# Kernel tuning notes

Hardware: AMD Instinct MI355X
Metric: run time of the kernel (lower is better)

## Reference

```python
import jax, jax.numpy as jnp
import numpy as np

NUM_HEADS = 16
KEY_DIM = 64
D_MODEL = 1024  # input feature dim


def setup_inputs() -> dict:
    key = jax.random.key(0)
    ks = jax.random.split(key, 10)
    B, T = 2, 2048
    s = 0.02
    return {
        "query": jax.random.normal(ks[0], (B, T, D_MODEL), jnp.float32),
        "Wq": jax.random.normal(ks[1], (D_MODEL, NUM_HEADS * KEY_DIM), jnp.float32) * s,
        "bq": jnp.zeros((NUM_HEADS * KEY_DIM,), jnp.float32),
        "Wk": jax.random.normal(ks[2], (D_MODEL, KEY_DIM), jnp.float32) * s,
        "bk": jnp.zeros((KEY_DIM,), jnp.float32),
        "Wv": jax.random.normal(ks[3], (D_MODEL, KEY_DIM), jnp.float32) * s,
        "bv": jnp.zeros((KEY_DIM,), jnp.float32),
        "Wo": jax.random.normal(ks[4], (NUM_HEADS * KEY_DIM, NUM_HEADS * KEY_DIM), jnp.float32) * s,
        "bo": jnp.zeros((NUM_HEADS * KEY_DIM,), jnp.float32),
    }


def reference(query, Wq, bq, Wk, bk, Wv, bv, Wo, bo):
    B, Tq, _ = query.shape
    # self-attention: key = value = query
    q = query @ Wq + bq                      # [B,Tq,H*D]
    k = query @ Wk + bk                      # [B,Tk,D] (single shared head)
    v = query @ Wv + bv                      # [B,Tk,D]
    q = q.reshape(B, Tq, NUM_HEADS, KEY_DIM)
    # scores: [B,H,Tq,Tk] — K broadcast across heads (MQA)
    scores = jnp.einsum("bqhd,bkd->bhqk", q, k) / jnp.sqrt(
        jnp.asarray(KEY_DIM, jnp.float32))
    attn = jax.nn.softmax(scores, axis=-1)
    out = jnp.einsum("bhqk,bkd->bqhd", attn, v)  # [B,Tq,H,D]
    out = out.reshape(B, Tq, NUM_HEADS * KEY_DIM)
    return out @ Wo + bo
```

## Files before the change

### kernel.cpp

```cpp
#include <hip/hip_runtime.h>
#include <math.h>

#define T_SEQ 2048
#define DM 1024
#define NH 16
#define KD 64
#define MTOT 4096

typedef __attribute__((ext_vector_type(16))) float f32x16;
typedef __attribute__((ext_vector_type(8))) __bf16 bf16x8;
typedef __attribute__((ext_vector_type(4))) __bf16 bf16x4;
typedef __attribute__((ext_vector_type(2))) __bf16 bf16x2;
typedef __attribute__((ext_vector_type(2))) int i32x2;

#define MFMA32 __builtin_amdgcn_mfma_f32_32x32x16_bf16

#define QSCALE 0.1803368801111f

__global__ void detect_dtype(const unsigned short* __restrict__ w, int* flag) {
  __shared__ int s;
  if (threadIdx.x == 0) s = 0;
  __syncthreads();
  int bad = 0;
  for (int i = threadIdx.x; i < 4096; i += blockDim.x) {
    unsigned e = (w[i] >> 7) & 0xFF;
    if (e >= 0xC0) bad = 1;
  }
  if (bad) atomicOr(&s, 1);
  __syncthreads();
  if (threadIdx.x == 0) *flag = s;
}

template <typename T> struct alignas(4 * sizeof(T)) V4T { T v[4]; };

template <typename T>
__device__ __forceinline__ float4 ld4f(const T* p) {
  V4T<T> g = *reinterpret_cast<const V4T<T>*>(p);
  return make_float4((float)g.v[0], (float)g.v[1], (float)g.v[2], (float)g.v[3]);
}

struct bf2 { __bf16 h, l; };
__device__ __forceinline__ bf2 split2(float v) {
  bf2 r;
  r.h = (__bf16)v;
  r.l = (__bf16)(v - (float)r.h);
  return r;
}

__device__ __forceinline__ unsigned pkbf(__bf16 a, __bf16 b) {
  bf16x2 t;
  t[0] = a;
  t[1] = b;
  return __builtin_bit_cast(unsigned, t);
}

__device__ __forceinline__ float fexp2(float x) {
#if __has_builtin(__builtin_amdgcn_exp2f)
  return __builtin_amdgcn_exp2f(x);
#else
  return __expf(0.69314718056f * x);
#endif
}

__device__ __forceinline__ void plswap(unsigned& a, unsigned& b) {
  i32x2 r = __builtin_amdgcn_permlane32_swap((int)a, (int)b, false, false);
  a = (unsigned)r[0];
  b = (unsigned)r[1];
}

__device__ __forceinline__ f32x16 zero16() {
  f32x16 z;
#pragma unroll
  for (int i = 0; i < 16; ++i) z[i] = 0.f;
  return z;
}

__device__ __forceinline__ int drow(int reg, int l5) {
  return (reg & 3) + 8 * (reg >> 2) + 4 * l5;
}

__device__ __forceinline__ void gload16(const void* g, void* l) {
  __builtin_amdgcn_global_load_lds(
      (const __attribute__((address_space(1))) unsigned int*)g,
      (__attribute__((address_space(3))) unsigned int*)l, 16, 0, 0);
}

__device__ __forceinline__ int swzc(int row, int c) {
  return (((((c >> 3) ^ row) & 7)) << 3) | (c & 7);
}

template <typename T, bool LO>
__global__ __launch_bounds__(256) void asplit(
    const int* __restrict__ flag, int want, const T* __restrict__ A,
    __bf16* __restrict__ Ah, __bf16* __restrict__ Al) {
  if (*flag != want) return;
  const int gid = blockIdx.x * 256 + threadIdx.x;
  const int row = gid >> 7;
  const int c0 = (gid & 127) * 8;
  float4 v0 = ld4f(A + (size_t)row * 1024 + c0);
  float4 v1 = ld4f(A + (size_t)row * 1024 + c0 + 4);
  float vv[8] = {v0.x, v0.y, v0.z, v0.w, v1.x, v1.y, v1.z, v1.w};
  bf16x8 h, lo;
#pragma unroll
  for (int j = 0; j < 8; ++j) {
    bf2 s = split2(vv[j]);
    h[j] = s.h;
    lo[j] = s.l;
  }
  const int cb = (c0 & ~63) | (swzc(row & 7, c0 & 63) & ~7);
  *reinterpret_cast<bf16x8*>(Ah + (size_t)row * 1024 + cb) = h;
  if (LO) *reinterpret_cast<bf16x8*>(Al + (size_t)row * 1024 + cb) = lo;
}

template <typename T, bool LO>
__global__ __launch_bounds__(256) void tsplit(
    const int* __restrict__ flag, int want, const T* __restrict__ W,
    __bf16* __restrict__ Th, __bf16* __restrict__ Tl, int K, int N) {
  if (*flag != want) return;
  __shared__ float ts[32][33];
  const int t = threadIdx.x;
  const int k0 = blockIdx.x * 32, n0 = blockIdx.y * 32;
#pragma unroll
  for (int i = 0; i < 4; ++i) {
    int idx = t + 256 * i;
    int r = idx >> 5, c = idx & 31;
    ts[r][c] = (float)W[(size_t)(k0 + r) * N + n0 + c];
  }
  __syncthreads();
#pragma unroll
  for (int i = 0; i < 4; ++i) {
    int idx = t + 256 * i;
    int r = idx >> 5, c = idx & 31;
    bf2 s = split2(ts[c][r]);
    const int rr = n0 + r, cc = k0 + c;
    const int sc = (cc & ~63) | swzc(rr & 7, cc & 63);
    Th[(size_t)rr * K + sc] = s.h;
    if (LO) Tl[(size_t)rr * K + sc] = s.l;
  }
}

template <typename T>
__global__ __launch_bounds__(256, 4) void gemmqkv(
    const int* __restrict__ flag, int want,
    const __bf16* __restrict__ Ah_g, const __bf16* __restrict__ Bh_g,
    const T* __restrict__ bq, const T* __restrict__ bk,
    const T* __restrict__ bv,
    __bf16* __restrict__ Qh, __bf16* __restrict__ Kh2,
    __bf16* __restrict__ Vh2) {
  if (*flag != want) return;
  __shared__ __bf16 As[128][64], Bs[128][64];
  const int t = threadIdx.x, l = t & 63, w = t >> 6;
  const int l31 = l & 31, l5 = l >> 5, l7 = l31 & 7;
  const int m0 = blockIdx.x * 128, n0 = blockIdx.y * 128;

  f32x16 acc[4];
#pragma unroll
  for (int nt = 0; nt < 4; ++nt) acc[nt] = zero16();

  for (int k0 = 0; k0 < 1024; k0 += 64) {
    __syncthreads();
#pragma unroll
    for (int i = 0; i < 4; ++i) {
      const int idx = i * 256 + t;
      const int rr = idx >> 3;
      const int c8 = (t & 7) * 8;
      gload16(Ah_g + (size_t)(m0 + rr) * 1024 + k0 + c8, (__bf16*)As + idx * 8);
      gload16(Bh_g + (size_t)(n0 + rr) * 1024 + k0 + c8, (__bf16*)Bs + idx * 8);
    }
    __syncthreads();
#pragma unroll
    for (int kb = 0; kb < 4; ++kb) {
      const int p = ((2 * kb + l5) ^ l7) * 8;
      bf16x8 ah = *reinterpret_cast<const bf16x8*>(&As[w * 32 + l31][p]);
#pragma unroll
      for (int nt = 0; nt < 4; ++nt) {
        bf16x8 bh = *reinterpret_cast<const bf16x8*>(&Bs[nt * 32 + l31][p]);
        acc[nt] = MFMA32(ah, bh, acc[nt], 0, 0, 0);
      }
    }
  }
#pragma unroll
  for (int nt = 0; nt < 4; ++nt) {
    const int cbase = n0 + nt * 32;
    const int col = cbase + l31;
    if (cbase < 1024) {
      const float bb = (float)bq[col];
#pragma unroll
      for (int reg = 0; reg < 16; ++reg) {
        const int mrow = m0 + w * 32 + drow(reg, l5);
        Qh[(size_t)mrow * 1024 + col] = (__bf16)((acc[nt][reg] + bb) * QSCALE);
      }
    } else if (cbase < 1088) {
      const int d = col - 1024;
      const float bb = (float)bk[d];
#pragma unroll
      for (int reg = 0; reg < 16; ++reg) {
        const int mrow = m0 + w * 32 + drow(reg, l5);
        Kh2[(size_t)mrow * 64 + swzc(mrow & 7, d)] = (__bf16)(acc[nt][reg] + bb);
      }
    } else {
      const int d = col - 1088;
      const float bb = (float)bv[d];
#pragma unroll
      for (int reg = 0; reg < 16; ++reg) {
        const int mrow = m0 + w * 32 + drow(reg, l5);
        const int bb2 = mrow >> 11, tt = mrow & 2047;
        const int sct = (tt & ~63) | swzc(d & 7, tt & 63);
        Vh2[((size_t)bb2 * 64 + d) * 2048 + sct] = (__bf16)(acc[nt][reg] + bb);
      }
    }
  }
}

template <typename T>
__global__ __launch_bounds__(256, 2) void gemmwo(
    const int* __restrict__ flag, int want,
    const __bf16* __restrict__ Ahi, const __bf16* __restrict__ Alo,
    const __bf16* __restrict__ Bh, const __bf16* __restrict__ Bl,
    const T* __restrict__ bias, T* __restrict__ CT) {
  if (*flag != want) return;
  __shared__ __bf16 Ah[128][64], Al[128][64];
  __shared__ __bf16 Bth[128][64], Btl[128][64];
  const int t = threadIdx.x, l = t & 63, w = t >> 6;
  const int l31 = l & 31, l5 = l >> 5, l7 = l31 & 7;
  const int m0 = blockIdx.x * 128, n0 = blockIdx.y * 128;

  f32x16 acc[4];
#pragma unroll
  for (int nt = 0; nt < 4; ++nt) acc[nt] = zero16();

  for (int k0 = 0; k0 < 1024; k0 += 64) {
    __syncthreads();
#pragma unroll
    for (int i = 0; i < 4; ++i) {
      const int idx = i * 256 + t;
      const int rr = idx >> 3;
      const int c8 = (t & 7) * 8;
      const size_t ga = (size_t)(m0 + rr) * 1024 + k0 + c8;
      gload16(Ahi + ga, (__bf16*)Ah + idx * 8);
      gload16(Alo + ga, (__bf16*)Al + idx * 8);
      const size_t gb = (size_t)(n0 + rr) * 1024 + k0 + c8;
      gload16(Bh + gb, (__bf16*)Bth + idx * 8);
      gload16(Bl + gb, (__bf16*)Btl + idx * 8);
    }
    __syncthreads();
#pragma unroll
    for (int kb = 0; kb < 4; ++kb) {
      const int p = ((2 * kb + l5) ^ l7) * 8;
      bf16x8 ah = *reinterpret_cast<const bf16x8*>(&Ah[w * 32 + l31][p]);
      bf16x8 al = *reinterpret_cast<const bf16x8*>(&Al[w * 32 + l31][p]);
#pragma unroll
      for (int nt = 0; nt < 4; ++nt) {
        bf16x8 bh = *reinterpret_cast<const bf16x8*>(&Bth[nt * 32 + l31][p]);
        bf16x8 bl = *reinterpret_cast<const bf16x8*>(&Btl[nt * 32 + l31][p]);
        acc[nt] = MFMA32(al, bh, acc[nt], 0, 0, 0);
        acc[nt] = MFMA32(ah, bl, acc[nt], 0, 0, 0);
        acc[nt] = MFMA32(ah, bh, acc[nt], 0, 0, 0);
      }
    }
  }
#pragma unroll
  for (int nt = 0; nt < 4; ++nt) {
    const int col = n0 + nt * 32 + l31;
    const float bb = (float)bias[col];
#pragma unroll
    for (int reg = 0; reg < 16; ++reg) {
      const int mrow = m0 + w * 32 + drow(reg, l5);
      CT[(size_t)mrow * 1024 + col] = (T)(acc[nt][reg] + bb);
    }
  }
}

template <typename T>
__global__ __launch_bounds__(512, 2) void attn8(
    const int* __restrict__ flag, int want,
    const __bf16* __restrict__ Qh_g, const __bf16* __restrict__ Kh_g,
    const __bf16* __restrict__ Vh_g,
    __bf16* __restrict__ AOhi, __bf16* __restrict__ AOlo) {
  if (*flag != want) return;
  __shared__ alignas(16) char arena[67584];
  const int t = threadIdx.x, l = t & 63, w = t >> 6;
  const int wq = w & 3, kvh = w >> 2;
  const int l31 = l & 31, l5 = l >> 5, l7 = l31 & 7;
  const int tl = t & 255;
  const int q0 = blockIdx.x * 256;
  const int h = blockIdx.y, b = blockIdx.z;

  __bf16* Kbase = (__bf16*)(arena + kvh * 16384);
  __bf16* Vbase = (__bf16*)(arena + 32768 + kvh * 16384);

  bf16x8 qh0[4], qh1[4];
  {
    const size_t qa = ((size_t)(b * T_SEQ + q0 + wq * 64 + l31)) * DM + h * KD;
#pragma unroll
    for (int ks = 0; ks < 4; ++ks) {
      qh0[ks] = *reinterpret_cast<const bf16x8*>(Qh_g + qa + ks * 16 + l5 * 8);
      qh1[ks] = *reinterpret_cast<const bf16x8*>(Qh_g + qa + (size_t)32 * DM + ks * 16 + l5 * 8);
    }
  }

  f32x16 o0 = zero16(), o1 = zero16(), o2 = zero16(), o3 = zero16();
  float lsa = 0.f, lsb = 0.f;

  const __bf16* Kg = Kh_g + (size_t)b * T_SEQ * KD;
  const __bf16* Vg = Vh_g + (size_t)b * KD * T_SEQ;
  const int sc8 = (tl & 7) * 8;
  const int kbase = kvh * 1024;

#define ASTAGE(BUF, KT0)                                                       \
  {                                                                            \
    const int r0 = tl >> 3, r1 = (256 + tl) >> 3;                              \
    gload16(Kg + (size_t)((KT0) + r0) * KD + sc8, Kbase + (BUF)*4096 + tl * 8);\
    gload16(Kg + (size_t)((KT0) + r1) * KD + sc8,                              \
            Kbase + (BUF)*4096 + (256 + tl) * 8);                              \
    gload16(Vg + (size_t)r0 * T_SEQ + (KT0) + sc8, Vbase + (BUF)*4096 + tl * 8);\
    gload16(Vg + (size_t)r1 * T_SEQ + (KT0) + sc8,                             \
            Vbase + (BUF)*4096 + (256 + tl) * 8);                              \
  }

  ASTAGE(0, kbase);
  __syncthreads();
  int cur = 0;

  for (int kt = 0; kt < 1024; kt += 64) {
    if (kt + 64 < 1024) ASTAGE(cur ^ 1, kbase + kt + 64);

    float rsa = 0.f, rsb = 0.f;
#pragma unroll
    for (int hf = 0; hf < 2; ++hf) {
      f32x16 sva = zero16(), svb = zero16();
#pragma unroll
      for (int ks = 0; ks < 4; ++ks) {
        const int p = ((2 * ks + l5) ^ l7) * 8;
        bf16x8 kh = *reinterpret_cast<const bf16x8*>(
            Kbase + cur * 4096 + (hf * 32 + l31) * 64 + p);
        sva = MFMA32(kh, qh0[ks], sva, 0, 0, 0);
        svb = MFMA32(kh, qh1[ks], svb, 0, 0, 0);
      }
      unsigned uha[8], uhb[8];
#pragma unroll
      for (int g2 = 0; g2 < 8; ++g2) {
        float a0 = fexp2(fminf(sva[2 * g2], 43.f));
        float a1 = fexp2(fminf(sva[2 * g2 + 1], 43.f));
        rsa += a0 + a1;
        uha[g2] = pkbf((__bf16)a0, (__bf16)a1);
        float b0 = fexp2(fminf(svb[2 * g2], 43.f));
        float b1 = fexp2(fminf(svb[2 * g2 + 1], 43.f));
        rsb += b0 + b1;
        uhb[g2] = pkbf((__bf16)b0, (__bf16)b1);
      }
#pragma unroll
      for (int kc = 0; kc < 2; ++kc) {
        unsigned a0 = uha[4 * kc], a1 = uha[4 * kc + 1];
        unsigned a2 = uha[4 * kc + 2], a3 = uha[4 * kc + 3];
        plswap(a0, a2);
        plswap(a1, a3);
        alignas(16) unsigned fa[4] = {a0, a1, a2, a3};
        bf16x8 pa = *reinterpret_cast<bf16x8*>(fa);
        unsigned b0 = uhb[4 * kc], b1 = uhb[4 * kc + 1];
        unsigned b2 = uhb[4 * kc + 2], b3 = uhb[4 * kc + 3];
        plswap(b0, b2);
        plswap(b1, b3);
        alignas(16) unsigned fb[4] = {b0, b1, b2, b3};
        bf16x8 pb = *reinterpret_cast<bf16x8*>(fb);

        const int kk = 2 * hf + kc;
        const int p = ((2 * kk + l5) ^ l7) * 8;
        bf16x8 v0 = *reinterpret_cast<const bf16x8*>(Vbase + cur * 4096 + l31 * 64 + p);
        bf16x8 v1 = *reinterpret_cast<const bf16x8*>(Vbase + cur * 4096 + (32 + l31) * 64 + p);
        o0 = MFMA32(pa, v0, o0, 0, 0, 0);
        o1 = MFMA32(pa, v1, o1, 0, 0, 0);
        o2 = MFMA32(pb, v0, o2, 0, 0, 0);
        o3 = MFMA32(pb, v1, o3, 0, 0, 0);
      }
    }
    {
      unsigned ra = __builtin_bit_cast(unsigned, rsa), rb = ra;
      plswap(ra, rb);
      lsa += __builtin_bit_cast(float, ra) + __builtin_bit_cast(float, rb);
      unsigned rc = __builtin_bit_cast(unsigned, rsb), rd = rc;
      plswap(rc, rd);
      lsb += __builtin_bit_cast(float, rc) + __builtin_bit_cast(float, rd);
    }
    __syncthreads();
    cur ^= 1;
  }

  float* ex = (float*)arena;
  float* exl = (float*)(arena + 65536);
  if (kvh == 1) {
#pragma unroll
    for (int g = 0; g < 4; ++g) {
      int cc0 = (0 + g + l) & 15;
      *reinterpret_cast<float4*>(&ex[((wq * 64 + l) << 6) + cc0 * 4]) =
          make_float4(o0[4 * g], o0[4 * g + 1], o0[4 * g + 2], o0[4 * g + 3]);
      int cc1 = (4 + g + l) & 15;
      *reinterpret_cast<float4*>(&ex[((wq * 64 + l) << 6) + cc1 * 4]) =
          make_float4(o1[4 * g], o1[4 * g + 1], o1[4 * g + 2], o1[4 * g + 3]);
      int cc2 = (8 + g + l) & 15;
      *reinterpret_cast<float4*>(&ex[((wq * 64 + l) << 6) + cc2 * 4]) =
          make_float4(o2[4 * g], o2[4 * g + 1], o2[4 * g + 2], o2[4 * g + 3]);
      int cc3 = (12 + g + l) & 15;
      *reinterpret_cast<float4*>(&ex[((wq * 64 + l) << 6) + cc3 * 4]) =
          make_float4(o3[4 * g], o3[4 * g + 1], o3[4 * g + 2], o3[4 * g + 3]);
    }
    exl[(wq * 64 + l) * 2] = lsa;
    exl[(wq * 64 + l) * 2 + 1] = lsb;
  }
  __syncthreads();
  if (kvh == 0) {
    lsa += exl[(wq * 64 + l) * 2];
    lsb += exl[(wq * 64 + l) * 2 + 1];
#pragma unroll
    for (int g = 0; g < 4; ++g) {
      int cc0 = (0 + g + l) & 15;
      float4 v = *reinterpret_cast<float4*>(&ex[((wq * 64 + l) << 6) + cc0 * 4]);
      o0[4 * g] += v.x; o0[4 * g + 1] += v.y; o0[4 * g + 2] += v.z; o0[4 * g + 3] += v.w;
      int cc1 = (4 + g + l) & 15;
      v = *reinterpret_cast<float4*>(&ex[((wq * 64 + l) << 6) + cc1 * 4]);
      o1[4 * g] += v.x; o1[4 * g + 1] += v.y; o1[4 * g + 2] += v.z; o1[4 * g + 3] += v.w;
      int cc2 = (8 + g + l) & 15;
      v = *reinterpret_cast<float4*>(&ex[((wq * 64 + l) << 6) + cc2 * 4]);
      o2[4 * g] += v.x; o2[4 * g + 1] += v.y; o2[4 * g + 2] += v.z; o2[4 * g + 3] += v.w;
      int cc3 = (12 + g + l) & 15;
      v = *reinterpret_cast<float4*>(&ex[((wq * 64 + l) << 6) + cc3 * 4]);
      o3[4 * g] += v.x; o3[4 * g + 1] += v.y; o3[4 * g + 2] += v.z; o3[4 * g + 3] += v.w;
    }
#pragma unroll
    for (int reg = 0; reg < 16; ++reg) {
      const int rq = drow(reg, l5);
      const int cl = ((((l31 >> 3) ^ rq) & 7) << 3) | (l31 & 7);
      const int ch = ((((4 + (l31 >> 3)) ^ rq) & 7) << 3) | (l31 & 7);
      const float inva = 1.f / __shfl(lsa, rq, 64);
      const size_t roa = ((size_t)(b * T_SEQ + q0 + wq * 64 + rq)) * DM + h * KD;
      bf2 s;
      s = split2(o0[reg] * inva); AOhi[roa + cl] = s.h; AOlo[roa + cl] = s.l;
      s = split2(o1[reg] * inva); AOhi[roa + ch] = s.h; AOlo[roa + ch] = s.l;
      const float invb = 1.f / __shfl(lsb, rq, 64);
      const size_t rob = roa + (size_t)32 * DM;
      s = split2(o2[reg] * invb); AOhi[rob + cl] = s.h; AOlo[rob + cl] = s.l;
      s = split2(o3[reg] * invb); AOhi[rob + ch] = s.h; AOlo[rob + ch] = s.l;
    }
  }
#undef ASTAGE
}

template <typename T>
static void run_pipeline(const int* flag, int want, void* const* d_in,
                         void* d_out, char* ws, size_t ws_size,
                         hipStream_t stream) {
  const T* query = (const T*)d_in[0];
  const T* Wq = (const T*)d_in[1];
  const T* bq = (const T*)d_in[2];
  const T* Wk = (const T*)d_in[3];
  const T* bk = (const T*)d_in[4];
  const T* Wv = (const T*)d_in[5];
  const T* bv = (const T*)d_in[6];
  const T* Wo = (const T*)d_in[7];
  const T* bo = (const T*)d_in[8];
  T* out = (T*)d_out;

  size_t o = 4096;
  __bf16* wqkvt_h = (__bf16*)(ws + o); o += (size_t)1152 * 1024 * 2;
  __bf16* wot_h = (__bf16*)(ws + o); o += 2097152;
  __bf16* wot_l = (__bf16*)(ws + o); o += 2097152;
  __bf16* khi = (__bf16*)(ws + o); o += 524288;
  __bf16* vthi = (__bf16*)(ws + o); o += 524288;
  __bf16* ahi = (__bf16*)(ws + o); o += 8388608;
  __bf16* alo = (__bf16*)(ws + o); o += 8388608;
  __bf16* aohi = ahi;
  __bf16* aolo = alo;
  __bf16* qhi;
  if (want == 1) {
    qhi = (__bf16*)d_out;
  } else {
    qhi = (__bf16*)(ws + o);
    o += 8388608;
  }

  asplit<T, false><<<(MTOT * DM) / (8 * 256), 256, 0, stream>>>(
      flag, want, query, ahi, nullptr);

  tsplit<T, false><<<dim3(32, 32), 256, 0, stream>>>(
      flag, want, Wq, wqkvt_h, nullptr, 1024, 1024);
  tsplit<T, false><<<dim3(32, 2), 256, 0, stream>>>(
      flag, want, Wk, wqkvt_h + (size_t)1024 * 1024, nullptr, 1024, 64);
  tsplit<T, false><<<dim3(32, 2), 256, 0, stream>>>(
      flag, want, Wv, wqkvt_h + (size_t)1088 * 1024, nullptr, 1024, 64);
  tsplit<T, true><<<dim3(32, 32), 256, 0, stream>>>(
      flag, want, Wo, wot_h, wot_l, 1024, 1024);

  gemmqkv<T><<<dim3(32, 9), 256, 0, stream>>>(
      flag, want, ahi, wqkvt_h, bq, bk, bv, qhi, khi, vthi);

  attn8<T><<<dim3(T_SEQ / 256, NH, 2), 512, 0, stream>>>(
      flag, want, qhi, khi, vthi, aohi, aolo);

  gemmwo<T><<<dim3(32, 8), 256, 0, stream>>>(
      flag, want, aohi, aolo, wot_h, wot_l, bo, out);
}

extern "C" void kernel_launch(void* const* d_in, const int* in_sizes, int n_in,
                              void* d_out, int out_size, void* d_ws, size_t ws_size,
                              hipStream_t stream) {
  char* ws = (char*)d_ws;
  int* flag = (int*)ws;

  detect_dtype<<<1, 256, 0, stream>>>((const unsigned short*)d_in[1], flag);
  run_pipeline<__bf16>(flag, 0, d_in, d_out, ws, ws_size, stream);
  run_pipeline<float>(flag, 1, d_in, d_out, ws, ws_size, stream);
}
```

Before: 215.3 us.

## Unify dtype pipelines, halve GEMM N-tiles, and compute softmax row sums via MFMA

Replaces the two templated pipelines with a single runtime-flag pipeline, so only one set of kernels launches and the dead early-exit launches disappear. The transpose-split launches for Wq/Wk/Wv/Wo merge into one kernel, and bias conversion moves into the detect kernel. The QKV and Wo GEMMs use 64-wide N tiles, doubling grid size for better CU fill. Attention now gets softmax denominators from extra MFMAs against a ones vector instead of scalar sums and lane swaps, and adds s_setprio around MFMA blocks. In exchange it adds MFMA work and more LDS in attention, which may lower occupancy.

```diff
diff --git a/kernel.cpp b/kernel.cpp
--- a/kernel.cpp
+++ b/kernel.cpp
@@ -9,35 +9,12 @@
 
 typedef __attribute__((ext_vector_type(16))) float f32x16;
 typedef __attribute__((ext_vector_type(8))) __bf16 bf16x8;
-typedef __attribute__((ext_vector_type(4))) __bf16 bf16x4;
 typedef __attribute__((ext_vector_type(2))) __bf16 bf16x2;
 typedef __attribute__((ext_vector_type(2))) int i32x2;
 
 #define MFMA32 __builtin_amdgcn_mfma_f32_32x32x16_bf16
 
 #define QSCALE 0.1803368801111f
-
-__global__ void detect_dtype(const unsigned short* __restrict__ w, int* flag) {
-  __shared__ int s;
-  if (threadIdx.x == 0) s = 0;
-  __syncthreads();
-  int bad = 0;
-  for (int i = threadIdx.x; i < 4096; i += blockDim.x) {
-    unsigned e = (w[i] >> 7) & 0xFF;
-    if (e >= 0xC0) bad = 1;
-  }
-  if (bad) atomicOr(&s, 1);
-  __syncthreads();
-  if (threadIdx.x == 0) *flag = s;
-}
-
-template <typename T> struct alignas(4 * sizeof(T)) V4T { T v[4]; };
-
-template <typename T>
-__device__ __forceinline__ float4 ld4f(const T* p) {
-  V4T<T> g = *reinterpret_cast<const V4T<T>*>(p);
-  return make_float4((float)g.v[0], (float)g.v[1], (float)g.v[2], (float)g.v[3]);
-}
 
 struct bf2 { __bf16 h, l; };
 __device__ __forceinline__ bf2 split2(float v) {
@@ -89,42 +66,82 @@
   return (((((c >> 3) ^ row) & 7)) << 3) | (c & 7);
 }
 
-template <typename T, bool LO>
-__global__ __launch_bounds__(256) void asplit(
-    const int* __restrict__ flag, int want, const T* __restrict__ A,
-    __bf16* __restrict__ Ah, __bf16* __restrict__ Al) {
-  if (*flag != want) return;
+__device__ __forceinline__ float ldf(const void* p, size_t i, int fl) {
+  return fl ? ((const float*)p)[i] : (float)(((const __bf16*)p)[i]);
+}
+
+__global__ void detect_prep(const unsigned short* __restrict__ w, int* flag,
+                            const void* bq, const void* bk, const void* bv,
+                            const void* bo, float* bqf, float* bkf,
+                            float* bvf, float* bof) {
+  __shared__ int s;
+  if (threadIdx.x == 0) s = 0;
+  __syncthreads();
+  int bad = 0;
+  for (int i = threadIdx.x; i < 4096; i += 256) {
+    unsigned e = (w[i] >> 7) & 0xFF;
+    if (e >= 0xC0) bad = 1;
+  }
+  if (bad) atomicOr(&s, 1);
+  __syncthreads();
+  const int fl = s;
+  if (threadIdx.x == 0) *flag = fl;
+  for (int i = threadIdx.x; i < 1024; i += 256) {
+    bqf[i] = ldf(bq, i, fl);
+    bof[i] = ldf(bo, i, fl);
+  }
+  if (threadIdx.x < 64) {
+    bkf[threadIdx.x] = ldf(bk, threadIdx.x, fl);
+    bvf[threadIdx.x] = ldf(bv, threadIdx.x, fl);
+  }
+}
+
+__global__ __launch_bounds__(256) void asplit_u(
+    const int* __restrict__ flag, const void* __restrict__ A,
+    __bf16* __restrict__ Ah) {
+  const int fl = *flag;
   const int gid = blockIdx.x * 256 + threadIdx.x;
   const int row = gid >> 7;
   const int c0 = (gid & 127) * 8;
-  float4 v0 = ld4f(A + (size_t)row * 1024 + c0);
-  float4 v1 = ld4f(A + (size_t)row * 1024 + c0 + 4);
-  float vv[8] = {v0.x, v0.y, v0.z, v0.w, v1.x, v1.y, v1.z, v1.w};
-  bf16x8 h, lo;
-#pragma unroll
-  for (int j = 0; j < 8; ++j) {
-    bf2 s = split2(vv[j]);
-    h[j] = s.h;
-    lo[j] = s.l;
+  bf16x8 h;
+  if (fl) {
+    const float* Af = (const float*)A + (size_t)row * 1024 + c0;
+    float4 v0 = *reinterpret_cast<const float4*>(Af);
+    float4 v1 = *reinterpret_cast<const float4*>(Af + 4);
+    h[0] = (__bf16)v0.x; h[1] = (__bf16)v0.y;
+    h[2] = (__bf16)v0.z; h[3] = (__bf16)v0.w;
+    h[4] = (__bf16)v1.x; h[5] = (__bf16)v1.y;
+    h[6] = (__bf16)v1.z; h[7] = (__bf16)v1.w;
+  } else {
+    h = *reinterpret_cast<const bf16x8*>((const __bf16*)A + (size_t)row * 1024 + c0);
   }
   const int cb = (c0 & ~63) | (swzc(row & 7, c0 & 63) & ~7);
   *reinterpret_cast<bf16x8*>(Ah + (size_t)row * 1024 + cb) = h;
-  if (LO) *reinterpret_cast<bf16x8*>(Al + (size_t)row * 1024 + cb) = lo;
-}
-
-template <typename T, bool LO>
-__global__ __launch_bounds__(256) void tsplit(
-    const int* __restrict__ flag, int want, const T* __restrict__ W,
-    __bf16* __restrict__ Th, __bf16* __restrict__ Tl, int K, int N) {
-  if (*flag != want) return;
+}
+
+__global__ __launch_bounds__(256) void tsplit_u(
+    const int* __restrict__ flag, const void* __restrict__ Wq,
+    const void* __restrict__ Wk, const void* __restrict__ Wv,
+    const void* __restrict__ Wo, __bf16* __restrict__ wqkv,
+    __bf16* __restrict__ woh, __bf16* __restrict__ wol) {
   __shared__ float ts[32][33];
+  const int fl = *flag;
   const int t = threadIdx.x;
-  const int k0 = blockIdx.x * 32, n0 = blockIdx.y * 32;
+  const int y = blockIdx.y;
+  const void* W;
+  int N, n0, rowoff;
+  bool lo = false;
+  __bf16* dh;
+  if (y < 32)      { W = Wq; N = 1024; n0 = y * 32;        rowoff = 0;    dh = wqkv; }
+  else if (y < 34) { W = Wk; N = 64;   n0 = (y - 32) * 32; rowoff = 1024; dh = wqkv; }
+  else if (y < 36) { W = Wv; N = 64;   n0 = (y - 34) * 32; rowoff = 1088; dh = wqkv; }
+  else             { W = Wo; N = 1024; n0 = (y - 36) * 32; rowoff = 0;    dh = woh; lo = true; }
+  const int k0 = blockIdx.x * 32;
 #pragma unroll
   for (int i = 0; i < 4; ++i) {
     int idx = t + 256 * i;
     int r = idx >> 5, c = idx & 31;
-    ts[r][c] = (float)W[(size_t)(k0 + r) * N + n0 + c];
+    ts[r][c] = ldf(W, (size_t)(k0 + r) * N + n0 + c, fl);
   }
   __syncthreads();
 #pragma unroll
@@ -132,40 +149,40 @@
     int idx = t + 256 * i;
     int r = idx >> 5, c = idx & 31;
     bf2 s = split2(ts[c][r]);
-    const int rr = n0 + r, cc = k0 + c;
+    const int rr = rowoff + n0 + r, cc = k0 + c;
     const int sc = (cc & ~63) | swzc(rr & 7, cc & 63);
-    Th[(size_t)rr * K + sc] = s.h;
-    if (LO) Tl[(size_t)rr * K + sc] = s.l;
-  }
-}
-
-template <typename T>
+    dh[(size_t)rr * 1024 + sc] = s.h;
+    if (lo) wol[(size_t)rr * 1024 + sc] = s.l;
+  }
+}
+
 __global__ __launch_bounds__(256, 4) void gemmqkv(
-    const int* __restrict__ flag, int want,
     const __bf16* __restrict__ Ah_g, const __bf16* __restrict__ Bh_g,
-    const T* __restrict__ bq, const T* __restrict__ bk,
-    const T* __restrict__ bv,
+    const float* __restrict__ bqf, const float* __restrict__ bkf,
+    const float* __restrict__ bvf,
     __bf16* __restrict__ Qh, __bf16* __restrict__ Kh2,
     __bf16* __restrict__ Vh2) {
-  if (*flag != want) return;
-  __shared__ __bf16 As[128][64], Bs[128][64];
+  __shared__ __bf16 As[128][64], Bs[64][64];
   const int t = threadIdx.x, l = t & 63, w = t >> 6;
   const int l31 = l & 31, l5 = l >> 5, l7 = l31 & 7;
-  const int m0 = blockIdx.x * 128, n0 = blockIdx.y * 128;
-
-  f32x16 acc[4];
-#pragma unroll
-  for (int nt = 0; nt < 4; ++nt) acc[nt] = zero16();
+  const int m0 = blockIdx.x * 128, n0 = blockIdx.y * 64;
+
+  f32x16 acc[2];
+  acc[0] = zero16();
+  acc[1] = zero16();
 
   for (int k0 = 0; k0 < 1024; k0 += 64) {
     __syncthreads();
+    const int c8 = (t & 7) * 8;
 #pragma unroll
     for (int i = 0; i < 4; ++i) {
       const int idx = i * 256 + t;
-      const int rr = idx >> 3;
-      const int c8 = (t & 7) * 8;
-      gload16(Ah_g + (size_t)(m0 + rr) * 1024 + k0 + c8, (__bf16*)As + idx * 8);
-      gload16(Bh_g + (size_t)(n0 + rr) * 1024 + k0 + c8, (__bf16*)Bs + idx * 8);
+      gload16(Ah_g + (size_t)(m0 + (idx >> 3)) * 1024 + k0 + c8, (__bf16*)As + idx * 8);
+    }
+#pragma unroll
+    for (int i = 0; i < 2; ++i) {
+      const int idx = i * 256 + t;
+      gload16(Bh_g + (size_t)(n0 + (idx >> 3)) * 1024 + k0 + c8, (__bf16*)Bs + idx * 8);
     }
     __syncthreads();
 #pragma unroll
@@ -173,18 +190,18 @@
       const int p = ((2 * kb + l5) ^ l7) * 8;
       bf16x8 ah = *reinterpret_cast<const bf16x8*>(&As[w * 32 + l31][p]);
 #pragma unroll
-      for (int nt = 0; nt < 4; ++nt) {
+      for (int nt = 0; nt < 2; ++nt) {
         bf16x8 bh = *reinterpret_cast<const bf16x8*>(&Bs[nt * 32 + l31][p]);
         acc[nt] = MFMA32(ah, bh, acc[nt], 0, 0, 0);
       }
     }
   }
 #pragma unroll
-  for (int nt = 0; nt < 4; ++nt) {
+  for (int nt = 0; nt < 2; ++nt) {
     const int cbase = n0 + nt * 32;
     const int col = cbase + l31;
     if (cbase < 1024) {
-      const float bb = (float)bq[col];
+      const float bb = bqf[col];
 #pragma unroll
       for (int reg = 0; reg < 16; ++reg) {
         const int mrow = m0 + w * 32 + drow(reg, l5);
@@ -192,7 +209,7 @@
       }
     } else if (cbase < 1088) {
       const int d = col - 1024;
-      const float bb = (float)bk[d];
+      const float bb = bkf[d];
 #pragma unroll
       for (int reg = 0; reg < 16; ++reg) {
         const int mrow = m0 + w * 32 + drow(reg, l5);
@@ -200,7 +217,7 @@
       }
     } else {
       const int d = col - 1088;
-      const float bb = (float)bv[d];
+      const float bb = bvf[d];
 #pragma unroll
       for (int reg = 0; reg < 16; ++reg) {
         const int mrow = m0 + w * 32 + drow(reg, l5);
@@ -212,34 +229,35 @@
   }
 }
 
-template <typename T>
 __global__ __launch_bounds__(256, 2) void gemmwo(
-    const int* __restrict__ flag, int want,
+    const int* __restrict__ flag,
     const __bf16* __restrict__ Ahi, const __bf16* __restrict__ Alo,
     const __bf16* __restrict__ Bh, const __bf16* __restrict__ Bl,
-    const T* __restrict__ bias, T* __restrict__ CT) {
-  if (*flag != want) return;
+    const float* __restrict__ bof, void* __restrict__ CT) {
   __shared__ __bf16 Ah[128][64], Al[128][64];
-  __shared__ __bf16 Bth[128][64], Btl[128][64];
+  __shared__ __bf16 Bth[64][64], Btl[64][64];
   const int t = threadIdx.x, l = t & 63, w = t >> 6;
   const int l31 = l & 31, l5 = l >> 5, l7 = l31 & 7;
-  const int m0 = blockIdx.x * 128, n0 = blockIdx.y * 128;
-
-  f32x16 acc[4];
-#pragma unroll
-  for (int nt = 0; nt < 4; ++nt) acc[nt] = zero16();
+  const int m0 = blockIdx.x * 128, n0 = blockIdx.y * 64;
+
+  f32x16 acc[2];
+  acc[0] = zero16();
+  acc[1] = zero16();
 
   for (int k0 = 0; k0 < 1024; k0 += 64) {
     __syncthreads();
+    const int c8 = (t & 7) * 8;
 #pragma unroll
     for (int i = 0; i < 4; ++i) {
       const int idx = i * 256 + t;
-      const int rr = idx >> 3;
-      const int c8 = (t & 7) * 8;
-      const size_t ga = (size_t)(m0 + rr) * 1024 + k0 + c8;
+      const size_t ga = (size_t)(m0 + (idx >> 3)) * 1024 + k0 + c8;
       gload16(Ahi + ga, (__bf16*)Ah + idx * 8);
       gload16(Alo + ga, (__bf16*)Al + idx * 8);
-      const size_t gb = (size_t)(n0 + rr) * 1024 + k0 + c8;
+    }
+#pragma unroll
+    for (int i = 0; i < 2; ++i) {
+      const int idx = i * 256 + t;
+      const size_t gb = (size_t)(n0 + (idx >> 3)) * 1024 + k0 + c8;
       gload16(Bh + gb, (__bf16*)Bth + idx * 8);
       gload16(Bl + gb, (__bf16*)Btl + idx * 8);
     }
@@ -250,7 +268,7 @@
       bf16x8 ah = *reinterpret_cast<const bf16x8*>(&Ah[w * 32 + l31][p]);
       bf16x8 al = *reinterpret_cast<const bf16x8*>(&Al[w * 32 + l31][p]);
 #pragma unroll
-      for (int nt = 0; nt < 4; ++nt) {
+      for (int nt = 0; nt < 2; ++nt) {
         bf16x8 bh = *reinterpret_cast<const bf16x8*>(&Bth[nt * 32 + l31][p]);
         bf16x8 bl = *reinterpret_cast<const bf16x8*>(&Btl[nt * 32 + l31][p]);
         acc[nt] = MFMA32(al, bh, acc[nt], 0, 0, 0);
@@ -259,26 +277,26 @@
       }
     }
   }
-#pragma unroll
-  for (int nt = 0; nt < 4; ++nt) {
+  const int fl = *flag;
+#pragma unroll
+  for (int nt = 0; nt < 2; ++nt) {
     const int col = n0 + nt * 32 + l31;
-    const float bb = (float)bias[col];
+    const float bb = bof[col];
 #pragma unroll
     for (int reg = 0; reg < 16; ++reg) {
       const int mrow = m0 + w * 32 + drow(reg, l5);
-      CT[(size_t)mrow * 1024 + col] = (T)(acc[nt][reg] + bb);
-    }
-  }
-}
-
-template <typename T>
+      const float v = acc[nt][reg] + bb;
+      if (fl) ((float*)CT)[(size_t)mrow * 1024 + col] = v;
+      else ((__bf16*)CT)[(size_t)mrow * 1024 + col] = (__bf16)v;
+    }
+  }
+}
+
 __global__ __launch_bounds__(512, 2) void attn8(
-    const int* __restrict__ flag, int want,
     const __bf16* __restrict__ Qh_g, const __bf16* __restrict__ Kh_g,
     const __bf16* __restrict__ Vh_g,
     __bf16* __restrict__ AOhi, __bf16* __restrict__ AOlo) {
-  if (*flag != want) return;
-  __shared__ alignas(16) char arena[67584];
+  __shared__ alignas(16) char arena[98304];
   const int t = threadIdx.x, l = t & 63, w = t >> 6;
   const int wq = w & 3, kvh = w >> 2;
   const int l31 = l & 31, l5 = l >> 5, l7 = l31 & 7;
@@ -289,6 +307,10 @@
   __bf16* Kbase = (__bf16*)(arena + kvh * 16384);
   __bf16* Vbase = (__bf16*)(arena + 32768 + kvh * 16384);
 
+  bf16x8 onesb;
+#pragma unroll
+  for (int j = 0; j < 8; ++j) onesb[j] = (__bf16)1.0f;
+
   bf16x8 qh0[4], qh1[4];
   {
     const size_t qa = ((size_t)(b * T_SEQ + q0 + wq * 64 + l31)) * DM + h * KD;
@@ -300,7 +322,7 @@
   }
 
   f32x16 o0 = zero16(), o1 = zero16(), o2 = zero16(), o3 = zero16();
-  float lsa = 0.f, lsb = 0.f;
+  f32x16 lacca = zero16(), laccb = zero16();
 
   const __bf16* Kg = Kh_g + (size_t)b * T_SEQ * KD;
   const __bf16* Vg = Vh_g + (size_t)b * KD * T_SEQ;
@@ -325,10 +347,10 @@
   for (int kt = 0; kt < 1024; kt += 64) {
     if (kt + 64 < 1024) ASTAGE(cur ^ 1, kbase + kt + 64);
 
-    float rsa = 0.f, rsb = 0.f;
 #pragma unroll
     for (int hf = 0; hf < 2; ++hf) {
       f32x16 sva = zero16(), svb = zero16();
+      __builtin_amdgcn_s_setprio(1);
 #pragma unroll
       for (int ks = 0; ks < 4; ++ks) {
         const int p = ((2 * ks + l5) ^ l7) * 8;
@@ -337,16 +359,15 @@
         sva = MFMA32(kh, qh0[ks], sva, 0, 0, 0);
         svb = MFMA32(kh, qh1[ks], svb, 0, 0, 0);
       }
+      __builtin_amdgcn_s_setprio(0);
       unsigned uha[8], uhb[8];
 #pragma unroll
       for (int g2 = 0; g2 < 8; ++g2) {
         float a0 = fexp2(fminf(sva[2 * g2], 43.f));
         float a1 = fexp2(fminf(sva[2 * g2 + 1], 43.f));
-        rsa += a0 + a1;
         uha[g2] = pkbf((__bf16)a0, (__bf16)a1);
         float b0 = fexp2(fminf(svb[2 * g2], 43.f));
         float b1 = fexp2(fminf(svb[2 * g2 + 1], 43.f));
-        rsb += b0 + b1;
         uhb[g2] = pkbf((__bf16)b0, (__bf16)b1);
       }
 #pragma unroll
@@ -368,19 +389,15 @@
         const int p = ((2 * kk + l5) ^ l7) * 8;
         bf16x8 v0 = *reinterpret_cast<const bf16x8*>(Vbase + cur * 4096 + l31 * 64 + p);
         bf16x8 v1 = *reinterpret_cast<const bf16x8*>(Vbase + cur * 4096 + (32 + l31) * 64 + p);
+        __builtin_amdgcn_s_setprio(1);
+        lacca = MFMA32(pa, onesb, lacca, 0, 0, 0);
         o0 = MFMA32(pa, v0, o0, 0, 0, 0);
         o1 = MFMA32(pa, v1, o1, 0, 0, 0);
+        laccb = MFMA32(pb, onesb, laccb, 0, 0, 0);
         o2 = MFMA32(pb, v0, o2, 0, 0, 0);
         o3 = MFMA32(pb, v1, o3, 0, 0, 0);
-      }
-    }
-    {
-      unsigned ra = __builtin_bit_cast(unsigned, rsa), rb = ra;
-      plswap(ra, rb);
-      lsa += __builtin_bit_cast(float, ra) + __builtin_bit_cast(float, rb);
-      unsigned rc = __builtin_bit_cast(unsigned, rsb), rd = rc;
-      plswap(rc, rd);
-      lsb += __builtin_bit_cast(float, rc) + __builtin_bit_cast(float, rd);
+        __builtin_amdgcn_s_setprio(0);
+      }
     }
     __syncthreads();
     cur ^= 1;
@@ -403,14 +420,16 @@
       int cc3 = (12 + g + l) & 15;
       *reinterpret_cast<float4*>(&ex[((wq * 64 + l) << 6) + cc3 * 4]) =
           make_float4(o3[4 * g], o3[4 * g + 1], o3[4 * g + 2], o3[4 * g + 3]);
-    }
-    exl[(wq * 64 + l) * 2] = lsa;
-    exl[(wq * 64 + l) * 2 + 1] = lsb;
+      int s0 = (g + l) & 7;
+      *reinterpret_cast<float4*>(&exl[((wq * 64 + l) << 5) + s0 * 4]) =
+          make_float4(lacca[4 * g], lacca[4 * g + 1], lacca[4 * g + 2], lacca[4 * g + 3]);
+      int s1 = (4 + g + l) & 7;
+      *reinterpret_cast<float4*>(&exl[((wq * 64 + l) << 5) + s1 * 4]) =
+          make_float4(laccb[4 * g], laccb[4 * g + 1], laccb[4 * g + 2], laccb[4 * g + 3]);
+    }
   }
   __syncthreads();
   if (kvh == 0) {
-    lsa += exl[(wq * 64 + l) * 2];
-    lsb += exl[(wq * 64 + l) * 2 + 1];
 #pragma unroll
     for (int g = 0; g < 4; ++g) {
       int cc0 = (0 + g + l) & 15;
@@ -425,18 +444,26 @@
       int cc3 = (12 + g + l) & 15;
       v = *reinterpret_cast<float4*>(&ex[((wq * 64 + l) << 6) + cc3 * 4]);
       o3[4 * g] += v.x; o3[4 * g + 1] += v.y; o3[4 * g + 2] += v.z; o3[4 * g + 3] += v.w;
+      int s0 = (g + l) & 7;
+      v = *reinterpret_cast<float4*>(&exl[((wq * 64 + l) << 5) + s0 * 4]);
+      lacca[4 * g] += v.x; lacca[4 * g + 1] += v.y;
+      lacca[4 * g + 2] += v.z; lacca[4 * g + 3] += v.w;
+      int s1 = (4 + g + l) & 7;
+      v = *reinterpret_cast<float4*>(&exl[((wq * 64 + l) << 5) + s1 * 4]);
+      laccb[4 * g] += v.x; laccb[4 * g + 1] += v.y;
+      laccb[4 * g + 2] += v.z; laccb[4 * g + 3] += v.w;
     }
 #pragma unroll
     for (int reg = 0; reg < 16; ++reg) {
       const int rq = drow(reg, l5);
       const int cl = ((((l31 >> 3) ^ rq) & 7) << 3) | (l31 & 7);
       const int ch = ((((4 + (l31 >> 3)) ^ rq) & 7) << 3) | (l31 & 7);
-      const float inva = 1.f / __shfl(lsa, rq, 64);
+      const float inva = 1.f / lacca[reg];
       const size_t roa = ((size_t)(b * T_SEQ + q0 + wq * 64 + rq)) * DM + h * KD;
       bf2 s;
       s = split2(o0[reg] * inva); AOhi[roa + cl] = s.h; AOlo[roa + cl] = s.l;
       s = split2(o1[reg] * inva); AOhi[roa + ch] = s.h; AOlo[roa + ch] = s.l;
-      const float invb = 1.f / __shfl(lsb, rq, 64);
+      const float invb = 1.f / laccb[reg];
       const size_t rob = roa + (size_t)32 * DM;
       s = split2(o2[reg] * invb); AOhi[rob + cl] = s.h; AOlo[rob + cl] = s.l;
       s = split2(o3[reg] * invb); AOhi[rob + ch] = s.h; AOlo[rob + ch] = s.l;
@@ -445,68 +472,36 @@
 #undef ASTAGE
 }
 
-template <typename T>
-static void run_pipeline(const int* flag, int want, void* const* d_in,
-                         void* d_out, char* ws, size_t ws_size,
-                         hipStream_t stream) {
-  const T* query = (const T*)d_in[0];
-  const T* Wq = (const T*)d_in[1];
-  const T* bq = (const T*)d_in[2];
-  const T* Wk = (const T*)d_in[3];
-  const T* bk = (const T*)d_in[4];
-  const T* Wv = (const T*)d_in[5];
-  const T* bv = (const T*)d_in[6];
-  const T* Wo = (const T*)d_in[7];
-  const T* bo = (const T*)d_in[8];
-  T* out = (T*)d_out;
-
+extern "C" void kernel_launch(void* const* d_in, const int* in_sizes, int n_in,
+                              void* d_out, int out_size, void* d_ws, size_t ws_size,
+                              hipStream_t stream) {
+  char* ws = (char*)d_ws;
+  int* flag = (int*)ws;
   size_t o = 4096;
+  float* bqf = (float*)(ws + o); o += 4096;
+  float* bkf = (float*)(ws + o); o += 4096;
+  float* bvf = (float*)(ws + o); o += 4096;
+  float* bof = (float*)(ws + o); o += 4096;
   __bf16* wqkvt_h = (__bf16*)(ws + o); o += (size_t)1152 * 1024 * 2;
   __bf16* wot_h = (__bf16*)(ws + o); o += 2097152;
   __bf16* wot_l = (__bf16*)(ws + o); o += 2097152;
   __bf16* khi = (__bf16*)(ws + o); o += 524288;
   __bf16* vthi = (__bf16*)(ws + o); o += 524288;
   __bf16* ahi = (__bf16*)(ws + o); o += 8388608;
-  __bf16* alo = (__bf16*)(ws + o); o += 8388608;
+  __bf16* aolo = (__bf16*)(ws + o); o += 8388608;
+  __bf16* qhi = (__bf16*)(ws + o); o += 8388608;
   __bf16* aohi = ahi;
-  __bf16* aolo = alo;
-  __bf16* qhi;
-  if (want == 1) {
-    qhi = (__bf16*)d_out;
-  } else {
-    qhi = (__bf16*)(ws + o);
-    o += 8388608;
-  }
-
-  asplit<T, false><<<(MTOT * DM) / (8 * 256), 256, 0, stream>>>(
-      flag, want, query, ahi, nullptr);
-
-  tsplit<T, false><<<dim3(32, 32), 256, 0, stream>>>(
-      flag, want, Wq, wqkvt_h, nullptr, 1024, 1024);
-  tsplit<T, false><<<dim3(32, 2), 256, 0, stream>>>(
-      flag, want, Wk, wqkvt_h + (size_t)1024 * 1024, nullptr, 1024, 64);
-  tsplit<T, false><<<dim3(32, 2), 256, 0, stream>>>(
-      flag, want, Wv, wqkvt_h + (size_t)1088 * 1024, nullptr, 1024, 64);
-  tsplit<T, true><<<dim3(32, 32), 256, 0, stream>>>(
-      flag, want, Wo, wot_h, wot_l, 1024, 1024);
-
-  gemmqkv<T><<<dim3(32, 9), 256, 0, stream>>>(
-      flag, want, ahi, wqkvt_h, bq, bk, bv, qhi, khi, vthi);
-
-  attn8<T><<<dim3(T_SEQ / 256, NH, 2), 512, 0, stream>>>(
-      flag, want, qhi, khi, vthi, aohi, aolo);
-
-  gemmwo<T><<<dim3(32, 8), 256, 0, stream>>>(
-      flag, want, aohi, aolo, wot_h, wot_l, bo, out);
-}
-
-extern "C" void kernel_launch(void* const* d_in, const int* in_sizes, int n_in,
-                              void* d_out, int out_size, void* d_ws, size_t ws_size,
-                              hipStream_t stream) {
-  char* ws = (char*)d_ws;
-  int* flag = (int*)ws;
-
-  detect_dtype<<<1, 256, 0, stream>>>((const unsigned short*)d_in[1], flag);
-  run_pipeline<__bf16>(flag, 0, d_in, d_out, ws, ws_size, stream);
-  run_pipeline<float>(flag, 1, d_in, d_out, ws, ws_size, stream);
-}
+
+  detect_prep<<<1, 256, 0, stream>>>(
+      (const unsigned short*)d_in[1], flag, d_in[2], d_in[4], d_in[6], d_in[8],
+      bqf, bkf, bvf, bof);
+  asplit_u<<<2048, 256, 0, stream>>>(flag, d_in[0], ahi);
+  tsplit_u<<<dim3(32, 68), 256, 0, stream>>>(
+      flag, d_in[1], d_in[3], d_in[5], d_in[7], wqkvt_h, wot_h, wot_l);
+  gemmqkv<<<dim3(32, 18), 256, 0, stream>>>(
+      ahi, wqkvt_h, bqf, bkf, bvf, qhi, khi, vthi);
+  attn8<<<dim3(T_SEQ / 256, NH, 2), 512, 0, stream>>>(
+      qhi, khi, vthi, aohi, aolo);
+  gemmwo<<<dim3(32, 16), 256, 0, stream>>>(
+      flag, aohi, aolo, wot_h, wot_l, bof, d_out);
+}
```

New measurement: 198.0 us. -8.0%, faster.
